# Performance work log

Hardware: AMD Instinct MI355X
Metric: run time of the kernel (lower is better)

The kernel has to match this reference:

```python
import jax, jax.numpy as jnp
import numpy as np

VEC, H, B, S = 768, 256, 64, 512


def setup_inputs() -> dict:
    key = jax.random.key(0)
    ks = jax.random.split(key, 8)
    sc = 0.02
    return {
        "output_1": jax.random.normal(ks[0], (B, S, VEC), dtype=jnp.float32),
        "output_2": jax.random.normal(ks[1], (B, S, VEC), dtype=jnp.float32),
        "mlp_w": jax.random.normal(ks[2], (H, VEC), dtype=jnp.float32) * sc,
        "mlp_b": jnp.zeros((H,), dtype=jnp.float32),
        "fd_w": jax.random.normal(ks[3], (H, 2 * H), dtype=jnp.float32) * sc,
        "fd_b": jnp.zeros((H,), dtype=jnp.float32),
        "ff_w": jax.random.normal(ks[4], (1, H), dtype=jnp.float32) * sc,
        "ff_b": jnp.zeros((1,), dtype=jnp.float32),
    }


def reference(output_1, output_2, mlp_w, mlp_b, fd_w, fd_b, ff_w, ff_b):
    # eval-mode forward of Bert_coss
    o1 = jax.nn.relu(output_1 @ mlp_w.T + mlp_b)        # [B,S,H]
    o2 = jax.nn.relu(output_2 @ mlp_w.T + mlp_b)        # [B,S,H]
    o1_doc = jnp.mean(o1, axis=1)                        # [B,H]
    o2_doc = jnp.mean(o2, axis=1)                        # [B,H]
    h = jax.nn.relu(jnp.concatenate([o1_doc, o2_doc], axis=1) @ fd_w.T + fd_b)
    out = jax.nn.sigmoid(jnp.squeeze(h @ ff_w.T + ff_b))  # [B]
    # append doc vectors as an extra token
    o1e = jnp.concatenate([o1, o1_doc[:, None, :]], axis=1)  # [B,S+1,H]
    o2e = jnp.concatenate([o2, o2_doc[:, None, :]], axis=1)  # [B,S+1,H]
    # graph_match: scores + softmax over dim=1; only last column is used downstream
    a = jnp.einsum('bsh,bth->bst', o1e, o2e)             # [B,S+1,S+1]
    a_x = jax.nn.softmax(a, axis=1)
    att = a_x[:, :, -1].T                                # [S+1,B]
    att = jnp.concatenate([att[:-1], out[None, :]], axis=0)  # [S+1,B]
    return att
```

## Files before the change

kernel.cpp:

```cpp
#include <hip/hip_runtime.h>
#include <hip/hip_bf16.h>
#include <math.h>

#define B_ 64
#define S_ 512
#define VEC_ 768
#define H_ 256
#define M_ (B_*S_)

typedef float floatx4 __attribute__((ext_vector_type(4)));
typedef __bf16 bf16x8 __attribute__((ext_vector_type(8)));
typedef __bf16 bf16x4 __attribute__((ext_vector_type(4)));

__global__ __launch_bounds__(256) void prep_kernel(
    const float* __restrict__ mlp_w, __bf16* __restrict__ wbf, float* __restrict__ sums)
{
  const int bid = blockIdx.x;
  if (bid < 192) {
    const int i = bid * 256 + threadIdx.x;
    const float4 v = ((const float4*)mlp_w)[i];
    bf16x4 b = { (__bf16)v.x, (__bf16)v.y, (__bf16)v.z, (__bf16)v.w };
    *(bf16x4*)&wbf[(size_t)i * 4] = b;
  } else {
    const int i = (bid - 192) * 256 + threadIdx.x;
    ((float4*)sums)[i] = make_float4(0.f, 0.f, 0.f, 0.f);
  }
}

#define CHUNKB_ 65536

__device__ __forceinline__ bf16x8 cvt8(float4 a, float4 b) {
  bf16x8 v;
  v[0] = (__bf16)a.x; v[1] = (__bf16)a.y; v[2] = (__bf16)a.z; v[3] = (__bf16)a.w;
  v[4] = (__bf16)b.x; v[5] = (__bf16)b.y; v[6] = (__bf16)b.z; v[7] = (__bf16)b.w;
  return v;
}

__global__ __launch_bounds__(1024, 4) void gemm_doc_kernel(
    const float* __restrict__ out1, const float* __restrict__ out2,
    const __bf16* __restrict__ wbf, const float* __restrict__ mlp_b,
    __bf16* __restrict__ o1, float* __restrict__ sum1, float* __restrict__ sum2)
{
  __shared__ __align__(16) char smem[2 * CHUNKB_];

  const int tensor = blockIdx.y;
  const float* __restrict__ A = tensor ? out2 : out1;
  float* __restrict__ dsum = tensor ? sum2 : sum1;

  const int m0 = blockIdx.x * 256;
  const int bidx = blockIdx.x >> 1;
  const int t = threadIdx.x;
  const int lane = t & 63;
  const int wave = t >> 6;
  const int q = lane >> 4;
  const int c = lane & 15;

  const float* Ap = A + (size_t)(m0 + wave * 16 + c) * VEC_ + q * 8;

  const int brow = t >> 2, bq = t & 3;
  const __bf16* Bsrc = wbf + (size_t)brow * VEC_ + bq * 32;
  char* Bdst = smem + brow * 256;

  floatx4 acc[16];
#pragma unroll
  for (int j = 0; j < 16; j++) acc[j] = (floatx4){0.f, 0.f, 0.f, 0.f};

  float4 aR[4][2];
  bf16x8 sR[4];

#define ALOAD(st) {                                                           \
    aR[(st) % 4][0] = *(const float4*)(Ap + (st) * 32);                       \
    aR[(st) % 4][1] = *(const float4*)(Ap + (st) * 32 + 4); }

#define BLOAD(kc) { _Pragma("unroll")                                         \
    for (int i_ = 0; i_ < 4; i_++)                                            \
      sR[i_] = *(const bf16x8*)(Bsrc + (kc) * 128 + i_ * 8); }

#define BWRITE(kc) { _Pragma("unroll")                                        \
    for (int i_ = 0; i_ < 4; i_++)                                            \
      *(bf16x8*)(Bdst + ((kc) & 1) * CHUNKB_ +                                \
                 (((bq * 4 + i_) ^ (brow & 7)) * 16)) = sR[i_]; }

#define KSTEP(st) {                                                           \
    if ((st) + 3 < 24) ALOAD((st) + 3)                                        \
    const bf16x8 af = cvt8(aR[(st) % 4][0], aR[(st) % 4][1]);                 \
    const char* bb = smem + (((st) >> 2) & 1) * CHUNKB_ + c * 256 +           \
                     (((((st) & 3) * 4 + q) ^ (c & 7)) * 16);                 \
    bf16x8 bfr[8];                                                            \
    _Pragma("unroll")                                                         \
    for (int j = 0; j < 8; j++) bfr[j] = *(const bf16x8*)(bb + j * 4096);     \
    _Pragma("unroll")                                                         \
    for (int j = 0; j < 8; j++)                                               \
      acc[j] = __builtin_amdgcn_mfma_f32_16x16x32_bf16(af, bfr[j], acc[j], 0, 0, 0); \
    _Pragma("unroll")                                                         \
    for (int j = 0; j < 8; j++) bfr[j] = *(const bf16x8*)(bb + 32768 + j * 4096); \
    _Pragma("unroll")                                                         \
    for (int j = 0; j < 8; j++)                                               \
      acc[8 + j] = __builtin_amdgcn_mfma_f32_16x16x32_bf16(af, bfr[j], acc[8 + j], 0, 0, 0); \
  }

#define BOUNDARY(cn) {                                                        \
    BWRITE((cn) + 1)                                                          \
    if ((cn) < 4) BLOAD((cn) + 2)                                             \
    asm volatile("s_waitcnt lgkmcnt(0)" ::: "memory");                        \
    __builtin_amdgcn_s_barrier(); }

  ALOAD(0) ALOAD(1) ALOAD(2)
  BLOAD(0)
  BWRITE(0)
  BLOAD(1)
  asm volatile("s_waitcnt lgkmcnt(0)" ::: "memory");
  __builtin_amdgcn_s_barrier();

  KSTEP(0)  KSTEP(1)  KSTEP(2)  KSTEP(3)  BOUNDARY(0)
  KSTEP(4)  KSTEP(5)  KSTEP(6)  KSTEP(7)  BOUNDARY(1)
  KSTEP(8)  KSTEP(9)  KSTEP(10) KSTEP(11) BOUNDARY(2)
  KSTEP(12) KSTEP(13) KSTEP(14) KSTEP(15) BOUNDARY(3)
  KSTEP(16) KSTEP(17) KSTEP(18) KSTEP(19) BOUNDARY(4)
  KSTEP(20) KSTEP(21) KSTEP(22) KSTEP(23)

#undef ALOAD
#undef BLOAD
#undef BWRITE
#undef KSTEP
#undef BOUNDARY

#pragma unroll
  for (int j = 0; j < 16; j++) {
    const int n = j * 16 + c;
    const float bias = mlp_b[n];
    float colsum = 0.f;
    const int mb = m0 + wave * 16 + q * 4;
#pragma unroll
    for (int r = 0; r < 4; r++) {
      float v = acc[j][r] + bias;
      v = fmaxf(v, 0.f);
      colsum += v;
      if (tensor == 0) o1[(size_t)(mb + r) * H_ + n] = (__bf16)v;
    }
    colsum += __shfl_down(colsum, 32);
    colsum += __shfl_down(colsum, 16);
    if (lane < 16)
      atomicAdd(&dsum[bidx * H_ + j * 16 + lane], colsum);
  }
}

__global__ __launch_bounds__(256) void logits_kernel(
    const __bf16* __restrict__ o1, const float* __restrict__ sum1,
    const float* __restrict__ sum2, float* __restrict__ lg)
{
  const int b = blockIdx.y;
  const int t = threadIdx.x, lane = t & 63, wave = t >> 6;
  const int s = blockIdx.x * 4 + wave;
  if (s > 512) return;
  const float sc = 1.f / 512.f;
  const float4 w4 = ((const float4*)&sum2[b * H_])[lane];
  float p;
  if (s < 512) {
    const bf16x4 x = ((const bf16x4*)&o1[((size_t)b * S_ + s) * H_])[lane];
    p = ((float)x[0] * w4.x + (float)x[1] * w4.y +
         (float)x[2] * w4.z + (float)x[3] * w4.w) * sc;
  } else {
    const float4 x = ((const float4*)&sum1[b * H_])[lane];
    p = (x.x * w4.x + x.y * w4.y + x.z * w4.z + x.w * w4.w) * sc * sc;
  }
  p += __shfl_down(p, 32); p += __shfl_down(p, 16); p += __shfl_down(p, 8);
  p += __shfl_down(p, 4);  p += __shfl_down(p, 2);  p += __shfl_down(p, 1);
  if (lane == 0) lg[b * 513 + s] = p;
}

__global__ __launch_bounds__(256) void softmax_head_kernel(
    const float* __restrict__ lg, const float* __restrict__ sum1, const float* __restrict__ sum2,
    const float* __restrict__ fd_w, const float* __restrict__ fd_b,
    const float* __restrict__ ff_w, const float* __restrict__ ff_b,
    float* __restrict__ out)
{
  const int b = blockIdx.x, t = threadIdx.x, lane = t & 63, wave = t >> 6;
  __shared__ __align__(16) float dc[512];
  __shared__ float sl[513];
  __shared__ float red[4], r1[4], r2[4];

  dc[t]       = sum1[b * H_ + t] * (1.f / 512.f);
  dc[t + 256] = sum2[b * H_ + t] * (1.f / 512.f);
  for (int i = t; i < 513; i += 256) sl[i] = lg[b * 513 + i];
  __syncthreads();
  const float4* wrow = (const float4*)&fd_w[(size_t)t * 512];
  const float4* dc4  = (const float4*)dc;
  float a0 = 0.f, a1 = 0.f;
#pragma unroll 8
  for (int k = 0; k < 128; k += 2) {
    const float4 w0 = wrow[k],     d0 = dc4[k];
    const float4 w1 = wrow[k + 1], d1 = dc4[k + 1];
    a0 += w0.x * d0.x + w0.y * d0.y + w0.z * d0.z + w0.w * d0.w;
    a1 += w1.x * d1.x + w1.y * d1.y + w1.z * d1.z + w1.w * d1.w;
  }
  const float h = fmaxf(a0 + a1 + fd_b[t], 0.f);
  float part = ff_w[t] * h;
  part += __shfl_down(part, 32); part += __shfl_down(part, 16);
  part += __shfl_down(part, 8);  part += __shfl_down(part, 4);
  part += __shfl_down(part, 2);  part += __shfl_down(part, 1);
  if (lane == 0) red[wave] = part;

  float m = -1e30f;
  for (int i = t; i < 513; i += 256) m = fmaxf(m, sl[i]);
  m = fmaxf(m, __shfl_down(m, 32)); m = fmaxf(m, __shfl_down(m, 16));
  m = fmaxf(m, __shfl_down(m, 8));  m = fmaxf(m, __shfl_down(m, 4));
  m = fmaxf(m, __shfl_down(m, 2));  m = fmaxf(m, __shfl_down(m, 1));
  if (lane == 0) r1[wave] = m;
  __syncthreads();
  m = fmaxf(fmaxf(r1[0], r1[1]), fmaxf(r1[2], r1[3]));
  float psum = 0.f;
  for (int i = t; i < 513; i += 256) { const float e = expf(sl[i] - m); sl[i] = e; psum += e; }
  psum += __shfl_down(psum, 32); psum += __shfl_down(psum, 16); psum += __shfl_down(psum, 8);
  psum += __shfl_down(psum, 4);  psum += __shfl_down(psum, 2);  psum += __shfl_down(psum, 1);
  if (lane == 0) r2[wave] = psum;
  __syncthreads();
  const float inv = 1.f / (r2[0] + r2[1] + r2[2] + r2[3]);
  for (int s = t; s < 512; s += 256) out[s * 64 + b] = sl[s] * inv;
  if (t == 0) {
    const float tot = red[0] + red[1] + red[2] + red[3] + ff_b[0];
    out[(size_t)512 * 64 + b] = 1.f / (1.f + expf(-tot));
  }
}

extern "C" void kernel_launch(void* const* d_in, const int* in_sizes, int n_in,
                              void* d_out, int out_size, void* d_ws, size_t ws_size,
                              hipStream_t stream) {
  const float* out1  = (const float*)d_in[0];
  const float* out2  = (const float*)d_in[1];
  const float* mlp_w = (const float*)d_in[2];
  const float* mlp_b = (const float*)d_in[3];
  const float* fd_w  = (const float*)d_in[4];
  const float* fd_b  = (const float*)d_in[5];
  const float* ff_w  = (const float*)d_in[6];
  const float* ff_b  = (const float*)d_in[7];
  float* out = (float*)d_out;

  __bf16* o1  = (__bf16*)d_ws;
  __bf16* wbf = o1 + (size_t)M_ * H_;
  float*  s1  = (float*)(wbf + (size_t)H_ * VEC_);
  float*  s2  = s1 + B_ * H_;
  float*  lgw = s2 + B_ * H_;

  prep_kernel<<<224, 256, 0, stream>>>(mlp_w, wbf, s1);
  gemm_doc_kernel<<<dim3(128, 2), 1024, 0, stream>>>(out1, out2, wbf, mlp_b, o1, s1, s2);
  logits_kernel<<<dim3(129, B_), 256, 0, stream>>>(o1, s1, s2, lgw);
  softmax_head_kernel<<<B_, 256, 0, stream>>>(lgw, s1, s2, fd_w, fd_b, ff_w, ff_b, out);
}
```

Before: 286.8 us.

## Retile GEMM waves to 32x128, batch logits rows, transpose fd_w for coalescing

The GEMM now assigns each wave a 32-row by 128-column tile instead of 16 by 256. This halves the LDS B-fragment reads per MFMA, at the cost of more A global loads per wave. The logits kernel processes 16 rows per wave with far fewer blocks, and the 513th entry is computed separately. fd_w is transposed in the prep kernel so the head's matrix-vector product reads weights coalesced across threads.

Result: slower. 414.3 us (+44.5%).

```diff
diff --git a/kernel.cpp b/kernel.cpp
--- a/kernel.cpp
+++ b/kernel.cpp
@@ -13,17 +13,27 @@
 typedef __bf16 bf16x4 __attribute__((ext_vector_type(4)));
 
 __global__ __launch_bounds__(256) void prep_kernel(
-    const float* __restrict__ mlp_w, __bf16* __restrict__ wbf, float* __restrict__ sums)
+    const float* __restrict__ mlp_w, const float* __restrict__ fd_w,
+    __bf16* __restrict__ wbf, float* __restrict__ sums, float* __restrict__ fd_wT)
 {
   const int bid = blockIdx.x;
+  const int t = threadIdx.x;
   if (bid < 192) {
-    const int i = bid * 256 + threadIdx.x;
+    const int i = bid * 256 + t;
     const float4 v = ((const float4*)mlp_w)[i];
     bf16x4 b = { (__bf16)v.x, (__bf16)v.y, (__bf16)v.z, (__bf16)v.w };
     *(bf16x4*)&wbf[(size_t)i * 4] = b;
+  } else if (bid < 224) {
+    const int i = (bid - 192) * 256 + t;
+    ((float4*)sums)[i] = make_float4(0.f, 0.f, 0.f, 0.f);
   } else {
-    const int i = (bid - 192) * 256 + threadIdx.x;
-    ((float4*)sums)[i] = make_float4(0.f, 0.f, 0.f, 0.f);
+    const int j0 = (bid - 224) * 4;
+#pragma unroll
+    for (int rr = 0; rr < 4; ++rr) {
+      const int j = j0 + rr;
+      for (int k = t; k < 512; k += 256)
+        fd_wT[(size_t)k * 256 + j] = fd_w[(size_t)j * 512 + k];
+    }
   }
 }
 
@@ -54,8 +64,10 @@
   const int wave = t >> 6;
   const int q = lane >> 4;
   const int c = lane & 15;
-
-  const float* Ap = A + (size_t)(m0 + wave * 16 + c) * VEC_ + q * 8;
+  const int wm = (wave >> 1) * 32;
+  const int wnb = (wave & 1) * 32768;
+
+  const float* Ap = A + (size_t)(m0 + wm + c) * VEC_ + q * 8;
 
   const int brow = t >> 2, bq = t & 3;
   const __bf16* Bsrc = wbf + (size_t)brow * VEC_ + bq * 32;
@@ -65,12 +77,14 @@
 #pragma unroll
   for (int j = 0; j < 16; j++) acc[j] = (floatx4){0.f, 0.f, 0.f, 0.f};
 
-  float4 aR[4][2];
+  float4 aR[3][4];
   bf16x8 sR[4];
 
 #define ALOAD(st) {                                                           \
-    aR[(st) % 4][0] = *(const float4*)(Ap + (st) * 32);                       \
-    aR[(st) % 4][1] = *(const float4*)(Ap + (st) * 32 + 4); }
+    aR[(st) % 3][0] = *(const float4*)(Ap + (st) * 32);                       \
+    aR[(st) % 3][1] = *(const float4*)(Ap + (st) * 32 + 4);                   \
+    aR[(st) % 3][2] = *(const float4*)(Ap + 16 * VEC_ + (st) * 32);           \
+    aR[(st) % 3][3] = *(const float4*)(Ap + 16 * VEC_ + (st) * 32 + 4); }
 
 #define BLOAD(kc) { _Pragma("unroll")                                         \
     for (int i_ = 0; i_ < 4; i_++)                                            \
@@ -82,21 +96,20 @@
                  (((bq * 4 + i_) ^ (brow & 7)) * 16)) = sR[i_]; }
 
 #define KSTEP(st) {                                                           \
+    const bf16x8 af0 = cvt8(aR[(st) % 3][0], aR[(st) % 3][1]);                \
+    const bf16x8 af1 = cvt8(aR[(st) % 3][2], aR[(st) % 3][3]);                \
     if ((st) + 3 < 24) ALOAD((st) + 3)                                        \
-    const bf16x8 af = cvt8(aR[(st) % 4][0], aR[(st) % 4][1]);                 \
-    const char* bb = smem + (((st) >> 2) & 1) * CHUNKB_ + c * 256 +           \
+    const char* bb = smem + (((st) >> 2) & 1) * CHUNKB_ + wnb + c * 256 +     \
                      (((((st) & 3) * 4 + q) ^ (c & 7)) * 16);                 \
     bf16x8 bfr[8];                                                            \
     _Pragma("unroll")                                                         \
     for (int j = 0; j < 8; j++) bfr[j] = *(const bf16x8*)(bb + j * 4096);     \
     _Pragma("unroll")                                                         \
     for (int j = 0; j < 8; j++)                                               \
-      acc[j] = __builtin_amdgcn_mfma_f32_16x16x32_bf16(af, bfr[j], acc[j], 0, 0, 0); \
-    _Pragma("unroll")                                                         \
-    for (int j = 0; j < 8; j++) bfr[j] = *(const bf16x8*)(bb + 32768 + j * 4096); \
+      acc[j] = __builtin_amdgcn_mfma_f32_16x16x32_bf16(af0, bfr[j], acc[j], 0, 0, 0); \
     _Pragma("unroll")                                                         \
     for (int j = 0; j < 8; j++)                                               \
-      acc[8 + j] = __builtin_amdgcn_mfma_f32_16x16x32_bf16(af, bfr[j], acc[8 + j], 0, 0, 0); \
+      acc[8 + j] = __builtin_amdgcn_mfma_f32_16x16x32_bf16(af1, bfr[j], acc[8 + j], 0, 0, 0); \
   }
 
 #define BOUNDARY(cn) {                                                        \
@@ -126,22 +139,25 @@
 #undef BOUNDARY
 
 #pragma unroll
-  for (int j = 0; j < 16; j++) {
-    const int n = j * 16 + c;
+  for (int j = 0; j < 8; j++) {
+    const int n = (wave & 1) * 128 + j * 16 + c;
     const float bias = mlp_b[n];
     float colsum = 0.f;
-    const int mb = m0 + wave * 16 + q * 4;
-#pragma unroll
-    for (int r = 0; r < 4; r++) {
-      float v = acc[j][r] + bias;
-      v = fmaxf(v, 0.f);
-      colsum += v;
-      if (tensor == 0) o1[(size_t)(mb + r) * H_ + n] = (__bf16)v;
+#pragma unroll
+    for (int i = 0; i < 2; i++) {
+      const int mb = m0 + wm + i * 16 + q * 4;
+#pragma unroll
+      for (int r = 0; r < 4; r++) {
+        float v = acc[i * 8 + j][r] + bias;
+        v = fmaxf(v, 0.f);
+        colsum += v;
+        if (tensor == 0) o1[(size_t)(mb + r) * H_ + n] = (__bf16)v;
+      }
     }
     colsum += __shfl_down(colsum, 32);
     colsum += __shfl_down(colsum, 16);
     if (lane < 16)
-      atomicAdd(&dsum[bidx * H_ + j * 16 + lane], colsum);
+      atomicAdd(&dsum[bidx * H_ + (wave & 1) * 128 + j * 16 + lane], colsum);
   }
 }
 
@@ -151,27 +167,31 @@
 {
   const int b = blockIdx.y;
   const int t = threadIdx.x, lane = t & 63, wave = t >> 6;
-  const int s = blockIdx.x * 4 + wave;
-  if (s > 512) return;
   const float sc = 1.f / 512.f;
   const float4 w4 = ((const float4*)&sum2[b * H_])[lane];
-  float p;
-  if (s < 512) {
+  const int sbase = blockIdx.x * 64 + wave * 16;
+#pragma unroll 4
+  for (int u = 0; u < 16; ++u) {
+    const int s = sbase + u;
     const bf16x4 x = ((const bf16x4*)&o1[((size_t)b * S_ + s) * H_])[lane];
-    p = ((float)x[0] * w4.x + (float)x[1] * w4.y +
-         (float)x[2] * w4.z + (float)x[3] * w4.w) * sc;
-  } else {
+    float p = ((float)x[0] * w4.x + (float)x[1] * w4.y +
+               (float)x[2] * w4.z + (float)x[3] * w4.w) * sc;
+    p += __shfl_down(p, 32); p += __shfl_down(p, 16); p += __shfl_down(p, 8);
+    p += __shfl_down(p, 4);  p += __shfl_down(p, 2);  p += __shfl_down(p, 1);
+    if (lane == 0) lg[b * 513 + s] = p;
+  }
+  if (blockIdx.x == 0 && wave == 0) {
     const float4 x = ((const float4*)&sum1[b * H_])[lane];
-    p = (x.x * w4.x + x.y * w4.y + x.z * w4.z + x.w * w4.w) * sc * sc;
-  }
-  p += __shfl_down(p, 32); p += __shfl_down(p, 16); p += __shfl_down(p, 8);
-  p += __shfl_down(p, 4);  p += __shfl_down(p, 2);  p += __shfl_down(p, 1);
-  if (lane == 0) lg[b * 513 + s] = p;
+    float p = (x.x * w4.x + x.y * w4.y + x.z * w4.z + x.w * w4.w) * sc * sc;
+    p += __shfl_down(p, 32); p += __shfl_down(p, 16); p += __shfl_down(p, 8);
+    p += __shfl_down(p, 4);  p += __shfl_down(p, 2);  p += __shfl_down(p, 1);
+    if (lane == 0) lg[b * 513 + 512] = p;
+  }
 }
 
 __global__ __launch_bounds__(256) void softmax_head_kernel(
     const float* __restrict__ lg, const float* __restrict__ sum1, const float* __restrict__ sum2,
-    const float* __restrict__ fd_w, const float* __restrict__ fd_b,
+    const float* __restrict__ fd_wT, const float* __restrict__ fd_b,
     const float* __restrict__ ff_w, const float* __restrict__ ff_b,
     float* __restrict__ out)
 {
@@ -184,17 +204,15 @@
   dc[t + 256] = sum2[b * H_ + t] * (1.f / 512.f);
   for (int i = t; i < 513; i += 256) sl[i] = lg[b * 513 + i];
   __syncthreads();
-  const float4* wrow = (const float4*)&fd_w[(size_t)t * 512];
-  const float4* dc4  = (const float4*)dc;
-  float a0 = 0.f, a1 = 0.f;
-#pragma unroll 8
-  for (int k = 0; k < 128; k += 2) {
-    const float4 w0 = wrow[k],     d0 = dc4[k];
-    const float4 w1 = wrow[k + 1], d1 = dc4[k + 1];
-    a0 += w0.x * d0.x + w0.y * d0.y + w0.z * d0.z + w0.w * d0.w;
-    a1 += w1.x * d1.x + w1.y * d1.y + w1.z * d1.z + w1.w * d1.w;
-  }
-  const float h = fmaxf(a0 + a1 + fd_b[t], 0.f);
+  float a0 = 0.f, a1 = 0.f, a2 = 0.f, a3 = 0.f;
+#pragma unroll 4
+  for (int k = 0; k < 512; k += 4) {
+    a0 += fd_wT[(size_t)(k + 0) * 256 + t] * dc[k + 0];
+    a1 += fd_wT[(size_t)(k + 1) * 256 + t] * dc[k + 1];
+    a2 += fd_wT[(size_t)(k + 2) * 256 + t] * dc[k + 2];
+    a3 += fd_wT[(size_t)(k + 3) * 256 + t] * dc[k + 3];
+  }
+  const float h = fmaxf((a0 + a1) + (a2 + a3) + fd_b[t], 0.f);
   float part = ff_w[t] * h;
   part += __shfl_down(part, 32); part += __shfl_down(part, 16);
   part += __shfl_down(part, 8);  part += __shfl_down(part, 4);
@@ -241,9 +259,10 @@
   float*  s1  = (float*)(wbf + (size_t)H_ * VEC_);
   float*  s2  = s1 + B_ * H_;
   float*  lgw = s2 + B_ * H_;
-
-  prep_kernel<<<224, 256, 0, stream>>>(mlp_w, wbf, s1);
+  float*  fwt = lgw + B_ * 513;
+
+  prep_kernel<<<288, 256, 0, stream>>>(mlp_w, fd_w, wbf, s1, fwt);
   gemm_doc_kernel<<<dim3(128, 2), 1024, 0, stream>>>(out1, out2, wbf, mlp_b, o1, s1, s2);
-  logits_kernel<<<dim3(129, B_), 256, 0, stream>>>(o1, s1, s2, lgw);
-  softmax_head_kernel<<<B_, 256, 0, stream>>>(lgw, s1, s2, fd_w, fd_b, ff_w, ff_b, out);
-}
+  logits_kernel<<<dim3(8, B_), 256, 0, stream>>>(o1, s1, s2, lgw);
+  softmax_head_kernel<<<B_, 256, 0, stream>>>(lgw, s1, s2, fwt, fd_b, ff_w, ff_b, out);
+}
```
